# Kernel tuning notes

Hardware: AMD Instinct MI355X
Metric: run time of the kernel (lower is better)

## Reference

```python
import jax, jax.numpy as jnp
import numpy as np

NUM_BEAMS = 2


def setup_inputs() -> dict:
    key = jax.random.key(0)
    ks = jax.random.split(key, 5)
    B, T, H, E, F = 128, 32, 768, 4, 3072
    x = jax.random.normal(ks[0], (B, T, H), dtype=jnp.float32)
    Wg = jax.random.normal(ks[1], (E, H), dtype=jnp.float32) * (1.0 / np.sqrt(H))
    W1 = jax.random.normal(ks[2], (E, H, F), dtype=jnp.float32) * (1.0 / np.sqrt(H))
    b1 = jnp.zeros((E, F), dtype=jnp.float32)
    W2 = jax.random.normal(ks[3], (E, F, H), dtype=jnp.float32) * (1.0 / np.sqrt(F))
    b2 = jnp.zeros((E, H), dtype=jnp.float32)
    return {"x": x, "Wg": Wg, "W1": W1, "b1": b1, "W2": W2, "b2": b2}


def reference(x, Wg, W1, b1, W2, b2):
    B, T, H = x.shape
    E = Wg.shape[0]
    nb = NUM_BEAMS
    # ---- forward_gate: mask is all-ones, so masked mean == mean over tokens ----
    x_avg = jnp.mean(x, axis=1)                          # [B, H]
    logits_gate = x_avg @ Wg.T                           # [B, E]
    prob_gate = jax.nn.softmax(logits_gate, axis=-1)     # [B, E]
    # ---- importance auxiliary loss (torch.std uses ddof=1) ----
    importance = jnp.sum(prob_gate, axis=0)              # [E]
    importance_loss = (jnp.std(importance, ddof=1) / jnp.mean(importance)) ** 2
    # ---- beam search, first layer: exp(log(p)) == p, top-k per row ----
    current_scores = jnp.exp(jnp.log(prob_gate))         # == prob_gate (kept for fidelity)
    topk_values, gate_idx = jax.lax.top_k(current_scores, nb)   # [B, nb]
    beam_scores = topk_values.reshape(nb * B)            # row-major flatten, matches .view
    expert_route = gate_idx.reshape(nb * B)[:, None]     # [B*nb, 1]
    beam_idx = jnp.arange(nb * B)
    current_expert_select = expert_route[:, -1]          # [B*nb]
    # ---- first layer: replicate x and scores along beam dim (interleaved) ----
    x_rep = jnp.repeat(x, nb, axis=0)                    # [B*nb, T, H]
    scores_rep = jnp.repeat(prob_gate, nb, axis=0)       # [B*nb, E]
    # input_x = x_rep[beam_idx] is identity here (beam_idx == arange)
    # ---- forward_expert_ffn: run ALL experts, mask+combine with gate prob ----
    h1 = jnp.einsum('bth,ehf->betf', x_rep, W1) + b1[None, :, None, :]
    h1 = jax.nn.gelu(h1, approximate=False)              # torch GELU is exact erf form
    cand = jnp.einsum('betf,efh->beth', h1, W2) + b2[None, :, None, :]  # [B*nb, E, T, H]
    weight = scores_rep * jax.nn.one_hot(current_expert_select, E, dtype=scores_rep.dtype)
    output = jnp.einsum('beth,be->bth', cand, weight)    # weighted sum over experts
    return output, beam_scores, expert_route, beam_idx, importance_loss
```

## Files before the change

### kernel.cpp

```cpp
#include <hip/hip_runtime.h>
#include <math.h>

typedef _Float16 f16;
typedef _Float16 f16x8 __attribute__((ext_vector_type(8)));
typedef float f32x4 __attribute__((ext_vector_type(4)));

#define Bn 128
#define Tn 32
#define Hn 768
#define En 4
#define Fn 3072
#define Rn 256

static constexpr size_t OUT_ELEMS  = (size_t)Rn*Tn*Hn;
static constexpr size_t SCORES_OFF = OUT_ELEMS;
static constexpr size_t ROUTE_OFF  = OUT_ELEMS + Rn;
static constexpr size_t BIDX_OFF   = OUT_ELEMS + 2*Rn;
static constexpr size_t LOSS_OFF   = OUT_ELEMS + 3*Rn;

#define WS_WSF    0u
#define WS_ROUTE  4096u
#define WS_GRP    8192u
#define WS_X16    16384u
#define WS_W1T    (WS_X16 + 2u*Bn*Tn*Hn)
#define WS_W2T    (WS_W1T + 2u*En*Hn*Fn)
#define WS_H1     (WS_W2T + 2u*En*Fn*Hn)

#define GLOAD16(g, l) __builtin_amdgcn_global_load_lds( \
    (const __attribute__((address_space(1))) unsigned int*)(g), \
    (__attribute__((address_space(3))) unsigned int*)(l), 16, 0, 0)

__device__ __forceinline__ float fast_gelu(float v) {
  float s = v * 0.70710678118f;
  float a = fabsf(s);
  float t = 1.0f / (1.0f + 0.3275911f * a);
  float y = t*(0.254829592f + t*(-0.284496736f + t*(1.421413741f +
            t*(-1.453152027f + t*1.061405429f))));
  float er = 1.0f - y * __expf(-a*a);
  er = (s < 0.0f) ? -er : er;
  return 0.5f * v * (1.0f + er);
}

__global__ __launch_bounds__(256) void gate_kernel(
    const float* __restrict__ x, const float* __restrict__ Wg,
    float* __restrict__ out, float* __restrict__ wsf, int* __restrict__ route,
    f16* __restrict__ x16)
{
  const int b = blockIdx.x;
  const int tid = threadIdx.x;
  const int w = tid >> 6, l = tid & 63;
  __shared__ float pacc[4][4];
  float a0=0.f, a1=0.f, a2=0.f, a3=0.f;
  const float* xb = x   + (size_t)b*Tn*Hn + (size_t)(w*8)*Hn;
  f16*         xh = x16 + (size_t)b*Tn*Hn + (size_t)(w*8)*Hn;
  #pragma unroll
  for (int k = 0; k < 12; ++k) {
    const int h = l + 64*k;
    const float w0 = Wg[0*Hn+h], w1 = Wg[1*Hn+h], w2 = Wg[2*Hn+h], w3 = Wg[3*Hn+h];
    #pragma unroll
    for (int t = 0; t < 8; ++t) {
      float v = xb[t*Hn + h];
      xh[t*Hn + h] = (f16)v;
      a0 += v*w0; a1 += v*w1; a2 += v*w2; a3 += v*w3;
    }
  }
  #pragma unroll
  for (int o = 32; o > 0; o >>= 1) {
    a0 += __shfl_down(a0,o); a1 += __shfl_down(a1,o);
    a2 += __shfl_down(a2,o); a3 += __shfl_down(a3,o);
  }
  if (l == 0) { pacc[w][0]=a0; pacc[w][1]=a1; pacc[w][2]=a2; pacc[w][3]=a3; }
  __syncthreads();
  if (tid == 0) {
    float lg[4];
    #pragma unroll
    for (int e = 0; e < 4; ++e)
      lg[e] = (pacc[0][e]+pacc[1][e]+pacc[2][e]+pacc[3][e]) * (1.0f/Tn);
    float m = fmaxf(fmaxf(lg[0],lg[1]), fmaxf(lg[2],lg[3]));
    float p[4]; float s = 0.f;
    #pragma unroll
    for (int e = 0; e < 4; ++e) { p[e] = expf(lg[e]-m); s += p[e]; }
    float inv = 1.f/s;
    #pragma unroll
    for (int e = 0; e < 4; ++e) { p[e] *= inv; wsf[b*4+e] = p[e]; }
    int i1 = 0;
    #pragma unroll
    for (int e = 1; e < 4; ++e) if (p[e] > p[i1]) i1 = e;
    int i2 = (i1 == 0) ? 1 : 0;
    #pragma unroll
    for (int e = 0; e < 4; ++e) if (e != i1 && p[e] > p[i2]) i2 = e;
    int idx[2] = {i1, i2};
    #pragma unroll
    for (int k = 0; k < 2; ++k) {
      int r = 2*b + k;
      float pv = p[idx[k]];
      wsf[512 + r] = pv;
      route[r] = idx[k];
      out[SCORES_OFF + r] = pv;
      out[ROUTE_OFF  + r] = (float)idx[k];
      out[BIDX_OFF   + r] = (float)r;
    }
  }
}

__global__ __launch_bounds__(64) void loss_kernel(
    const float* __restrict__ wsf, float* __restrict__ out)
{
  const int l = threadIdx.x;
  float i0=0.f,i1=0.f,i2=0.f,i3=0.f;
  for (int b = l; b < Bn; b += 64) {
    i0 += wsf[b*4+0]; i1 += wsf[b*4+1]; i2 += wsf[b*4+2]; i3 += wsf[b*4+3];
  }
  #pragma unroll
  for (int o = 32; o > 0; o >>= 1) {
    i0 += __shfl_down(i0,o); i1 += __shfl_down(i1,o);
    i2 += __shfl_down(i2,o); i3 += __shfl_down(i3,o);
  }
  if (l == 0) {
    float mean = 0.25f*(i0+i1+i2+i3);
    float d0=i0-mean, d1=i1-mean, d2=i2-mean, d3=i3-mean;
    float var = (d0*d0+d1*d1+d2*d2+d3*d3) * (1.f/3.f);
    out[LOSS_OFF] = var / (mean*mean);
  }
}

__global__ __launch_bounds__(64) void group_kernel(
    const int* __restrict__ route, int* __restrict__ grp)
{
  const int l = threadIdx.x;
  int cnt = 0;
  if (l < 4) { for (int r = 0; r < Rn; ++r) cnt += (route[r] == l); }
  int c0 = __shfl(cnt, 0), c1 = __shfl(cnt, 1), c2 = __shfl(cnt, 2), c3 = __shfl(cnt, 3);
  int off = (l >= 1 ? c0 : 0) + (l >= 2 ? c1 : 0) + (l >= 3 ? c2 : 0);
  if (l < 4) {
    int p = off;
    for (int r = 0; r < Rn; ++r) if (route[r] == l) grp[384 + p++] = r;
  }
  if (l == 0) {
    int cs[4] = {c0, c1, c2, c3};
    int os[4] = {0, c0, c0+c1, c0+c1+c2};
    int nt4 = 0;
    for (int e = 0; e < 4; ++e) {
      for (int s = 0; s < cs[e]; s += 4) {
        int nb = cs[e] - s; if (nb > 4) nb = 4;
        grp[8+nt4*3+0] = e; grp[8+nt4*3+1] = os[e]+s; grp[8+nt4*3+2] = nb;
        ++nt4;
      }
    }
    grp[0] = nt4;
  }
}

__global__ __launch_bounds__(256) void transcvt_kernel(
    const float* __restrict__ W1s, const float* __restrict__ W2s,
    f16* __restrict__ d1, f16* __restrict__ d2)
{
  __shared__ f16 t[64][74];
  int bid = blockIdx.x;
  const float* s; f16* d; int R, C, rc;
  if (bid < 2304) { s = W1s; d = d1; R = Hn; C = Fn; rc = bid; }
  else            { s = W2s; d = d2; R = Fn; C = Hn; rc = bid - 2304; }
  const int e = rc / 576; rc -= e*576;
  const int nx = C >> 6;
  const int cy = rc / nx, cx = rc - cy*nx;
  const int r0 = cy*64, c0 = cx*64;
  s += (size_t)e*R*C;
  d += (size_t)e*R*C;
  const int tid = threadIdx.x;
  const int i  = tid >> 2;
  const int j0 = (tid & 3) * 16;
  #pragma unroll
  for (int q = 0; q < 16; q += 4) {
    float4 v = *(const float4*)(s + (size_t)(r0+i)*C + c0 + j0 + q);
    t[i][j0+q+0]=(f16)v.x; t[i][j0+q+1]=(f16)v.y; t[i][j0+q+2]=(f16)v.z; t[i][j0+q+3]=(f16)v.w;
  }
  __syncthreads();
  f16 o[16];
  #pragma unroll
  for (int q = 0; q < 16; ++q) o[q] = t[j0+q][i];
  *(uint4*)(d + (size_t)(c0+i)*R + r0 + j0)     = *(uint4*)&o[0];
  *(uint4*)(d + (size_t)(c0+i)*R + r0 + j0 + 8) = *(uint4*)&o[8];
}

template<int KD, int ND, int BN, int NWAVE, int NBUF, bool G1>
__global__ __launch_bounds__(NWAVE*64, 2) void gemm_kernel(
    const f16* __restrict__ A16, const f16* __restrict__ B16,
    const float* __restrict__ bias, f16* __restrict__ oh,
    float* __restrict__ of, const int* __restrict__ grp,
    const float* __restrict__ wsf)
{
  constexpr int NWY  = BN / 64;
  constexpr int NY   = ND / BN;
  constexpr int NT   = KD / 64;
  constexpr int GL_A = 1024 / (NWAVE*64);
  constexpr int GL_B = (BN*8) / (NWAVE*64);
  constexpr int NLD  = GL_A + GL_B;
  constexpr int BUFSZ = (128 + BN) * 128;
  constexpr int PRE_D = NBUF - 1;
  constexpr int TPR  = NWAVE*2;
  static_assert(NT % NBUF == 0, "NT % NBUF");

  const int ntiles = grp[0];
  const int njobs  = ntiles * NY;
  const int tid  = threadIdx.x;
  const int lane = tid & 63;
  const int w    = tid >> 6;

  extern __shared__ __align__(16) char smem[];

  const int wm = w / NWY, wn = w % NWY;
  const int lr = lane & 15, lk = lane >> 4;
  const int rowA0 = wm*64;
  const int rowB0 = wn*64;
  const int r7 = lr & 7;
  const int ub[2] = { ((lk) ^ r7) << 4, ((4+lk) ^ r7) << 4 };

  const int j0 = (int)(((long long)blockIdx.x     * njobs) / gridDim.x);
  const int j1 = (int)(((long long)(blockIdx.x+1) * njobs) / gridDim.x);

  for (int job = j0; job < j1; ++job) {
    const int tix = job / NY;
    const int ny  = job - tix*NY;
    const int e      = grp[8+tix*3+0];
    const int bstart = grp[8+tix*3+1];
    const int nb     = grp[8+tix*3+2];
    const int n0     = ny * BN;

    const f16* asrc[GL_A];
    #pragma unroll
    for (int i = 0; i < GL_A; ++i) {
      const int U   = (w*GL_A + i)*64 + lane;
      const int row = U >> 3;
      const int gu  = (U & 7) ^ (row & 7);
      int slot = row >> 5; if (slot >= nb) slot = nb - 1;
      const int beam = grp[384 + bstart + slot];
      const size_t rbase = (G1 ? (size_t)(beam>>1)*Tn : (size_t)beam*Tn) + (row & 31);
      asrc[i] = A16 + rbase*(size_t)KD + gu*8;
    }
    const f16* bsrc[GL_B];
    #pragma unroll
    for (int i = 0; i < GL_B; ++i) {
      const int U   = (w*GL_B + i)*64 + lane;
      const int row = U >> 3;
      const int gu  = (U & 7) ^ (row & 7);
      bsrc[i] = B16 + (size_t)e*ND*KD + (size_t)(n0 + row)*KD + gu*8;
    }

    f32x4 acc[4][4];
    #pragma unroll
    for (int i=0;i<4;++i)
      #pragma unroll
      for (int j=0;j<4;++j) acc[i][j] = (f32x4){0.f,0.f,0.f,0.f};

    auto STAGE = [&](int bsel, int kt2) {
      char* Ad = smem + bsel*BUFSZ + (w*GL_A)*1024;
      #pragma unroll
      for (int i = 0; i < GL_A; ++i) GLOAD16(asrc[i] + kt2*64, Ad + i*1024);
      char* Bd = smem + bsel*BUFSZ + 128*128 + (w*GL_B)*1024;
      #pragma unroll
      for (int i = 0; i < GL_B; ++i) GLOAD16(bsrc[i] + kt2*64, Bd + i*1024);
    };

#define PHASE(BUFI, KS, PRE, POST) do {                                        \
      const char* Ab_ = smem + (BUFI)*BUFSZ;                                   \
      const char* Bb_ = Ab_ + 128*128;                                         \
      f16x8 af[4], bf[4];                                                      \
      _Pragma("unroll")                                                        \
      for (int mi=0;mi<4;++mi)                                                 \
        af[mi] = *(const f16x8*)(Ab_ + (rowA0+mi*16+lr)*128 + ub[KS]);         \
      _Pragma("unroll")                                                        \
      for (int ni=0;ni<4;++ni)                                                 \
        bf[ni] = *(const f16x8*)(Bb_ + (rowB0+ni*16+lr)*128 + ub[KS]);         \
      PRE;                                                                     \
      __builtin_amdgcn_s_barrier();                                            \
      __builtin_amdgcn_sched_barrier(0);                                       \
      asm volatile("s_waitcnt lgkmcnt(0)" ::: "memory");                       \
      __builtin_amdgcn_sched_barrier(0);                                       \
      __builtin_amdgcn_s_setprio(1);                                           \
      _Pragma("unroll")                                                        \
      for (int mi=0;mi<4;++mi)                                                 \
        _Pragma("unroll")                                                      \
        for (int ni=0;ni<4;++ni)                                               \
          acc[mi][ni] = __builtin_amdgcn_mfma_f32_16x16x32_f16(af[mi], bf[ni], acc[mi][ni], 0, 0, 0); \
      __builtin_amdgcn_s_setprio(0);                                           \
      POST;                                                                    \
      __builtin_amdgcn_s_barrier();                                            \
      __builtin_amdgcn_sched_barrier(0);                                       \
    } while (0)

#define TILE(BUFI, KT) do {                                                    \
      PHASE(BUFI, 0,                                                           \
            { if ((KT)+PRE_D < NT) STAGE(((BUFI)+PRE_D)%NBUF, (KT)+PRE_D); },  \
            {});                                                               \
      PHASE(BUFI, 1, {},                                                       \
            { if (PRE_D == 2 && (KT)+2 < NT) {                                 \
                asm volatile("s_waitcnt vmcnt(%0)" :: "i"(NLD) : "memory");    \
              } else if ((KT)+1 < NT) {                                        \
                asm volatile("s_waitcnt vmcnt(0)" ::: "memory");               \
              }                                                                \
              __builtin_amdgcn_sched_barrier(0); });                           \
    } while (0)

    STAGE(0, 0);
    if (PRE_D == 2) {
      STAGE(1, 1);
      asm volatile("s_waitcnt vmcnt(%0)" :: "i"(NLD) : "memory");
    } else {
      asm volatile("s_waitcnt vmcnt(0)" ::: "memory");
    }
    __builtin_amdgcn_sched_barrier(0);
    __builtin_amdgcn_s_barrier();
    __builtin_amdgcn_sched_barrier(0);

    if constexpr (NBUF == 3) {
      for (int kt = 0; kt < NT; kt += 3) {
        TILE(0, kt);
        TILE(1, kt+1);
        TILE(2, kt+2);
      }
    } else {
      for (int kt = 0; kt < NT; kt += 2) {
        TILE(0, kt);
        TILE(1, kt+1);
      }
    }
#undef TILE
#undef PHASE

    const int nvalid = nb * Tn;
    char* cst = smem;
    float bvals[4];
    if (G1) {
      #pragma unroll
      for (int ni=0;ni<4;++ni) bvals[ni] = bias[e*ND + n0 + rowB0 + ni*16 + lr];
    }
    #pragma unroll
    for (int mi=0;mi<4;++mi){
      #pragma unroll
      for (int j=0;j<4;++j){
        const int m = rowA0 + mi*16 + (lane>>4)*4 + j;
        const int m7 = m & 7;
        #pragma unroll
        for (int ni=0;ni<4;++ni){
          const int n = rowB0 + ni*16 + lr;
          if (G1) {
            float v = acc[mi][ni][j] + bvals[ni];
            *(f16*)(cst + m*512 + (((n>>3)^m7)<<4) + (n&7)*2) = (f16)fast_gelu(v);
          } else {
            *(float*)(cst + m*512 + (((n>>2)^m7)<<4) + (n&3)*4) = acc[mi][ni][j];
          }
        }
      }
    }
    __syncthreads();
    {
      const int u  = tid & 31;
      const int tr = tid >> 5;
      float4 b4;
      if (!G1) b4 = *(const float4*)(bias + e*ND + n0 + u*4);
      #pragma unroll
      for (int it = 0; it < 128/TPR; ++it) {
        const int rl = it*TPR + tr;
        if (rl < nvalid) {
          const int beam = grp[384 + bstart + (rl>>5)];
          if (G1) {
            uint4 v = *(const uint4*)(cst + rl*512 + (((u&24)|((u&7)^(rl&7)))<<4));
            *(uint4*)(oh + ((size_t)beam*Tn + (rl&31))*(size_t)ND + n0 + u*8) = v;
          } else {
            const float sc = wsf[512 + beam];
            float4 v = *(const float4*)(cst + rl*512 + (((u&24)|((u&7)^(rl&7)))<<4));
            v.x = (v.x + b4.x)*sc; v.y = (v.y + b4.y)*sc;
            v.z = (v.z + b4.z)*sc; v.w = (v.w + b4.w)*sc;
            *(float4*)(of + ((size_t)beam*Tn + (rl&31))*(size_t)Hn + n0 + u*4) = v;
          }
        }
      }
    }
    __syncthreads();
  }
}

extern "C" void kernel_launch(void* const* d_in, const int* in_sizes, int n_in,
                              void* d_out, int out_size, void* d_ws, size_t ws_size,
                              hipStream_t stream)
{
  const float* x  = (const float*)d_in[0];
  const float* Wg = (const float*)d_in[1];
  const float* W1 = (const float*)d_in[2];
  const float* b1 = (const float*)d_in[3];
  const float* W2 = (const float*)d_in[4];
  const float* b2 = (const float*)d_in[5];
  float* out = (float*)d_out;
  char* ws = (char*)d_ws;
  float* wsf  = (float*)(ws + WS_WSF);
  int*   route= (int*)(ws + WS_ROUTE);
  int*   grp  = (int*)(ws + WS_GRP);
  f16*   x16  = (f16*)(ws + WS_X16);
  f16*   w1t  = (f16*)(ws + WS_W1T);
  f16*   w2t  = (f16*)(ws + WS_W2T);
  f16*   h1   = (f16*)(ws + WS_H1);

  gate_kernel<<<Bn, 256, 0, stream>>>(x, Wg, out, wsf, route, x16);
  group_kernel<<<1, 64, 0, stream>>>(route, grp);
  loss_kernel<<<1, 64, 0, stream>>>(wsf, out);
  transcvt_kernel<<<4608, 256, 0, stream>>>(W1, W2, w1t, w2t);

  auto g1 = gemm_kernel<Hn, Fn, 256, 8, 3, true>;
  auto g2 = gemm_kernel<Fn, Hn, 128, 4, 2, false>;
  const int sm1 = 3 * (128 + 256) * 128;
  const int sm2 = 2 * (128 + 128) * 128;
  hipFuncSetAttribute((const void*)g1, hipFuncAttributeMaxDynamicSharedMemorySize, sm1);
  hipFuncSetAttribute((const void*)g2, hipFuncAttributeMaxDynamicSharedMemorySize, sm2);
  g1<<<256, 512, sm1, stream>>>(x16, w1t, b1, h1, nullptr, grp, wsf);
  g2<<<512, 256, sm2, stream>>>(h1, w2t, b2, nullptr, out, grp, wsf);
}
```

Before: 231.8 us.

## Shrink GEMM K-tile to 32, drop persistent loop, one block per tile job

Both expert GEMMs now use a K step of 32 instead of 64, with a single-phase triple-buffered pipeline and a new XOR swizzle matched to 64-byte rows. Per-stage shared memory becomes much smaller, and G1's launch bounds request 4 blocks per CU to raise occupancy. The persistent job loop is replaced by a grid sized to the maximum tile count, with blocks past the real tile count exiting early. The trade-off is twice as many barriers and waits per K loop and a few idle blocks.

```diff
diff --git a/kernel.cpp b/kernel.cpp
--- a/kernel.cpp
+++ b/kernel.cpp
@@ -11,6 +11,7 @@
 #define En 4
 #define Fn 3072
 #define Rn 256
+#define MAXT4 67
 
 static constexpr size_t OUT_ELEMS  = (size_t)Rn*Tn*Hn;
 static constexpr size_t SCORES_OFF = OUT_ELEMS;
@@ -182,8 +183,8 @@
   *(uint4*)(d + (size_t)(c0+i)*R + r0 + j0 + 8) = *(uint4*)&o[8];
 }
 
-template<int KD, int ND, int BN, int NWAVE, int NBUF, bool G1>
-__global__ __launch_bounds__(NWAVE*64, 2) void gemm_kernel(
+template<int KD, int ND, int BN, int NWAVE, bool G1>
+__global__ __launch_bounds__(NWAVE*64, G1 ? 4 : 2) void gemm_kernel(
     const f16* __restrict__ A16, const f16* __restrict__ B16,
     const float* __restrict__ bias, f16* __restrict__ oh,
     float* __restrict__ of, const int* __restrict__ grp,
@@ -191,192 +192,166 @@
 {
   constexpr int NWY  = BN / 64;
   constexpr int NY   = ND / BN;
-  constexpr int NT   = KD / 64;
-  constexpr int GL_A = 1024 / (NWAVE*64);
-  constexpr int GL_B = (BN*8) / (NWAVE*64);
+  constexpr int NT   = KD / 32;
+  constexpr int NTHR = NWAVE * 64;
+  constexpr int GL_A = 512 / NTHR;
+  constexpr int GL_B = (BN*4) / NTHR;
   constexpr int NLD  = GL_A + GL_B;
-  constexpr int BUFSZ = (128 + BN) * 128;
-  constexpr int PRE_D = NBUF - 1;
-  constexpr int TPR  = NWAVE*2;
-  static_assert(NT % NBUF == 0, "NT % NBUF");
+  constexpr int BUFSZ = 8192 + BN*64;
+  constexpr int TPR  = NWAVE * 2;
+  static_assert(NT % 3 == 0, "NT%3");
 
   const int ntiles = grp[0];
-  const int njobs  = ntiles * NY;
-  const int tid  = threadIdx.x;
-  const int lane = tid & 63;
-  const int w    = tid >> 6;
+  const int tix = blockIdx.x / NY;
+  const int ny  = blockIdx.x % NY;
+  if (tix >= ntiles) return;
+  const int e      = grp[8+tix*3+0];
+  const int bstart = grp[8+tix*3+1];
+  const int nb     = grp[8+tix*3+2];
+  const int n0     = ny * BN;
+  const int tid    = threadIdx.x;
+  const int lane   = tid & 63;
+  const int w      = tid >> 6;
 
   extern __shared__ __align__(16) char smem[];
+
+  const f16* asrc[GL_A];
+  #pragma unroll
+  for (int i = 0; i < GL_A; ++i) {
+    const int U   = w*(GL_A*64) + i*64 + lane;
+    const int row = U >> 2;
+    const int gu  = (U & 3) ^ ((U >> 3) & 3);
+    int slot = row >> 5; if (slot >= nb) slot = nb - 1;
+    const int beam = grp[384 + bstart + slot];
+    const size_t rbase = (G1 ? (size_t)(beam>>1)*Tn : (size_t)beam*Tn) + (row & 31);
+    asrc[i] = A16 + rbase*(size_t)KD + gu*8;
+  }
+  const f16* bsrc[GL_B];
+  #pragma unroll
+  for (int i = 0; i < GL_B; ++i) {
+    const int U   = w*(GL_B*64) + i*64 + lane;
+    const int row = U >> 2;
+    const int gu  = (U & 3) ^ ((U >> 3) & 3);
+    bsrc[i] = B16 + (size_t)e*ND*KD + (size_t)(n0 + row)*KD + gu*8;
+  }
 
   const int wm = w / NWY, wn = w % NWY;
   const int lr = lane & 15, lk = lane >> 4;
   const int rowA0 = wm*64;
   const int rowB0 = wn*64;
-  const int r7 = lr & 7;
-  const int ub[2] = { ((lk) ^ r7) << 4, ((4+lk) ^ r7) << 4 };
-
-  const int j0 = (int)(((long long)blockIdx.x     * njobs) / gridDim.x);
-  const int j1 = (int)(((long long)(blockIdx.x+1) * njobs) / gridDim.x);
-
-  for (int job = j0; job < j1; ++job) {
-    const int tix = job / NY;
-    const int ny  = job - tix*NY;
-    const int e      = grp[8+tix*3+0];
-    const int bstart = grp[8+tix*3+1];
-    const int nb     = grp[8+tix*3+2];
-    const int n0     = ny * BN;
-
-    const f16* asrc[GL_A];
-    #pragma unroll
-    for (int i = 0; i < GL_A; ++i) {
-      const int U   = (w*GL_A + i)*64 + lane;
-      const int row = U >> 3;
-      const int gu  = (U & 7) ^ (row & 7);
-      int slot = row >> 5; if (slot >= nb) slot = nb - 1;
-      const int beam = grp[384 + bstart + slot];
-      const size_t rbase = (G1 ? (size_t)(beam>>1)*Tn : (size_t)beam*Tn) + (row & 31);
-      asrc[i] = A16 + rbase*(size_t)KD + gu*8;
-    }
-    const f16* bsrc[GL_B];
-    #pragma unroll
-    for (int i = 0; i < GL_B; ++i) {
-      const int U   = (w*GL_B + i)*64 + lane;
-      const int row = U >> 3;
-      const int gu  = (U & 7) ^ (row & 7);
-      bsrc[i] = B16 + (size_t)e*ND*KD + (size_t)(n0 + row)*KD + gu*8;
-    }
-
-    f32x4 acc[4][4];
-    #pragma unroll
-    for (int i=0;i<4;++i)
+  const int ub = (lk ^ ((lr >> 1) & 3)) << 4;
+
+  f32x4 acc[4][4];
+  #pragma unroll
+  for (int i=0;i<4;++i)
+    #pragma unroll
+    for (int j=0;j<4;++j) acc[i][j] = (f32x4){0.f,0.f,0.f,0.f};
+
+  auto STAGE = [&](int bsel, int kt2) {
+    char* Ad = smem + bsel*BUFSZ + (w*(GL_A*64))*16;
+    #pragma unroll
+    for (int i = 0; i < GL_A; ++i) GLOAD16(asrc[i] + kt2*32, Ad + i*1024);
+    char* Bd = smem + bsel*BUFSZ + 8192 + (w*(GL_B*64))*16;
+    #pragma unroll
+    for (int i = 0; i < GL_B; ++i) GLOAD16(bsrc[i] + kt2*32, Bd + i*1024);
+  };
+
+  auto TILE = [&](int k, int b, bool dost, int vmc) {
+    const char* Ab = smem + b*BUFSZ;
+    const char* Bb = Ab + 8192;
+    f16x8 af[4], bf[4];
+    #pragma unroll
+    for (int mi=0;mi<4;++mi)
+      af[mi] = *(const f16x8*)(Ab + (rowA0 + mi*16 + lr)*64 + ub);
+    #pragma unroll
+    for (int ni=0;ni<4;++ni)
+      bf[ni] = *(const f16x8*)(Bb + (rowB0 + ni*16 + lr)*64 + ub);
+    if (dost) STAGE((b+2)%3, k+2);
+    __builtin_amdgcn_sched_barrier(0);
+    __builtin_amdgcn_s_barrier();
+    __builtin_amdgcn_sched_barrier(0);
+    asm volatile("s_waitcnt lgkmcnt(0)" ::: "memory");
+    __builtin_amdgcn_sched_barrier(0);
+    __builtin_amdgcn_s_setprio(1);
+    #pragma unroll
+    for (int mi=0;mi<4;++mi)
       #pragma unroll
-      for (int j=0;j<4;++j) acc[i][j] = (f32x4){0.f,0.f,0.f,0.f};
-
-    auto STAGE = [&](int bsel, int kt2) {
-      char* Ad = smem + bsel*BUFSZ + (w*GL_A)*1024;
+      for (int ni=0;ni<4;++ni)
+        acc[mi][ni] = __builtin_amdgcn_mfma_f32_16x16x32_f16(af[mi], bf[ni], acc[mi][ni], 0, 0, 0);
+    __builtin_amdgcn_s_setprio(0);
+    if (vmc > 0)       asm volatile("s_waitcnt vmcnt(%0)" :: "i"(NLD) : "memory");
+    else if (vmc == 0) asm volatile("s_waitcnt vmcnt(0)" ::: "memory");
+    __builtin_amdgcn_sched_barrier(0);
+    __builtin_amdgcn_s_barrier();
+    __builtin_amdgcn_sched_barrier(0);
+  };
+
+  STAGE(0, 0);
+  STAGE(1, 1);
+  asm volatile("s_waitcnt vmcnt(%0)" :: "i"(NLD) : "memory");
+  __builtin_amdgcn_sched_barrier(0);
+  __builtin_amdgcn_s_barrier();
+  __builtin_amdgcn_sched_barrier(0);
+
+  {
+    int b = 0;
+    for (int k = 0; k < NT-2; ++k) {
+      TILE(k, b, true, NLD);
+      b = (b+1)%3;
+    }
+    TILE(NT-2, b, false, 0);
+    b = (b+1)%3;
+    TILE(NT-1, b, false, -1);
+  }
+
+  const int nvalid = nb * Tn;
+  char* cst = smem;
+  float bvals[4];
+  if (G1) {
+    #pragma unroll
+    for (int ni=0;ni<4;++ni) bvals[ni] = bias[e*ND + n0 + rowB0 + ni*16 + lr];
+  }
+  #pragma unroll
+  for (int mi=0;mi<4;++mi){
+    #pragma unroll
+    for (int j=0;j<4;++j){
+      const int m = rowA0 + mi*16 + (lane>>4)*4 + j;
+      const int m7 = m & 7;
       #pragma unroll
-      for (int i = 0; i < GL_A; ++i) GLOAD16(asrc[i] + kt2*64, Ad + i*1024);
-      char* Bd = smem + bsel*BUFSZ + 128*128 + (w*GL_B)*1024;
-      #pragma unroll
-      for (int i = 0; i < GL_B; ++i) GLOAD16(bsrc[i] + kt2*64, Bd + i*1024);
-    };
-
-#define PHASE(BUFI, KS, PRE, POST) do {                                        \
-      const char* Ab_ = smem + (BUFI)*BUFSZ;                                   \
-      const char* Bb_ = Ab_ + 128*128;                                         \
-      f16x8 af[4], bf[4];                                                      \
-      _Pragma("unroll")                                                        \
-      for (int mi=0;mi<4;++mi)                                                 \
-        af[mi] = *(const f16x8*)(Ab_ + (rowA0+mi*16+lr)*128 + ub[KS]);         \
-      _Pragma("unroll")                                                        \
-      for (int ni=0;ni<4;++ni)                                                 \
-        bf[ni] = *(const f16x8*)(Bb_ + (rowB0+ni*16+lr)*128 + ub[KS]);         \
-      PRE;                                                                     \
-      __builtin_amdgcn_s_barrier();                                            \
-      __builtin_amdgcn_sched_barrier(0);                                       \
-      asm volatile("s_waitcnt lgkmcnt(0)" ::: "memory");                       \
-      __builtin_amdgcn_sched_barrier(0);                                       \
-      __builtin_amdgcn_s_setprio(1);                                           \
-      _Pragma("unroll")                                                        \
-      for (int mi=0;mi<4;++mi)                                                 \
-        _Pragma("unroll")                                                      \
-        for (int ni=0;ni<4;++ni)                                               \
-          acc[mi][ni] = __builtin_amdgcn_mfma_f32_16x16x32_f16(af[mi], bf[ni], acc[mi][ni], 0, 0, 0); \
-      __builtin_amdgcn_s_setprio(0);                                           \
-      POST;                                                                    \
-      __builtin_amdgcn_s_barrier();                                            \
-      __builtin_amdgcn_sched_barrier(0);                                       \
-    } while (0)
-
-#define TILE(BUFI, KT) do {                                                    \
-      PHASE(BUFI, 0,                                                           \
-            { if ((KT)+PRE_D < NT) STAGE(((BUFI)+PRE_D)%NBUF, (KT)+PRE_D); },  \
-            {});                                                               \
-      PHASE(BUFI, 1, {},                                                       \
-            { if (PRE_D == 2 && (KT)+2 < NT) {                                 \
-                asm volatile("s_waitcnt vmcnt(%0)" :: "i"(NLD) : "memory");    \
-              } else if ((KT)+1 < NT) {                                        \
-                asm volatile("s_waitcnt vmcnt(0)" ::: "memory");               \
-              }                                                                \
-              __builtin_amdgcn_sched_barrier(0); });                           \
-    } while (0)
-
-    STAGE(0, 0);
-    if (PRE_D == 2) {
-      STAGE(1, 1);
-      asm volatile("s_waitcnt vmcnt(%0)" :: "i"(NLD) : "memory");
-    } else {
-      asm volatile("s_waitcnt vmcnt(0)" ::: "memory");
-    }
-    __builtin_amdgcn_sched_barrier(0);
-    __builtin_amdgcn_s_barrier();
-    __builtin_amdgcn_sched_barrier(0);
-
-    if constexpr (NBUF == 3) {
-      for (int kt = 0; kt < NT; kt += 3) {
-        TILE(0, kt);
-        TILE(1, kt+1);
-        TILE(2, kt+2);
-      }
-    } else {
-      for (int kt = 0; kt < NT; kt += 2) {
-        TILE(0, kt);
-        TILE(1, kt+1);
-      }
-    }
-#undef TILE
-#undef PHASE
-
-    const int nvalid = nb * Tn;
-    char* cst = smem;
-    float bvals[4];
-    if (G1) {
-      #pragma unroll
-      for (int ni=0;ni<4;++ni) bvals[ni] = bias[e*ND + n0 + rowB0 + ni*16 + lr];
-    }
-    #pragma unroll
-    for (int mi=0;mi<4;++mi){
-      #pragma unroll
-      for (int j=0;j<4;++j){
-        const int m = rowA0 + mi*16 + (lane>>4)*4 + j;
-        const int m7 = m & 7;
-        #pragma unroll
-        for (int ni=0;ni<4;++ni){
-          const int n = rowB0 + ni*16 + lr;
-          if (G1) {
-            float v = acc[mi][ni][j] + bvals[ni];
-            *(f16*)(cst + m*512 + (((n>>3)^m7)<<4) + (n&7)*2) = (f16)fast_gelu(v);
-          } else {
-            *(float*)(cst + m*512 + (((n>>2)^m7)<<4) + (n&3)*4) = acc[mi][ni][j];
-          }
+      for (int ni=0;ni<4;++ni){
+        const int n = rowB0 + ni*16 + lr;
+        if (G1) {
+          float v = acc[mi][ni][j] + bvals[ni];
+          *(f16*)(cst + m*512 + (((n>>3)^m7)<<4) + (n&7)*2) = (f16)fast_gelu(v);
+        } else {
+          *(float*)(cst + m*512 + (((n>>2)^m7)<<4) + (n&3)*4) = acc[mi][ni][j];
         }
       }
     }
-    __syncthreads();
-    {
-      const int u  = tid & 31;
-      const int tr = tid >> 5;
-      float4 b4;
-      if (!G1) b4 = *(const float4*)(bias + e*ND + n0 + u*4);
-      #pragma unroll
-      for (int it = 0; it < 128/TPR; ++it) {
-        const int rl = it*TPR + tr;
-        if (rl < nvalid) {
-          const int beam = grp[384 + bstart + (rl>>5)];
-          if (G1) {
-            uint4 v = *(const uint4*)(cst + rl*512 + (((u&24)|((u&7)^(rl&7)))<<4));
-            *(uint4*)(oh + ((size_t)beam*Tn + (rl&31))*(size_t)ND + n0 + u*8) = v;
-          } else {
-            const float sc = wsf[512 + beam];
-            float4 v = *(const float4*)(cst + rl*512 + (((u&24)|((u&7)^(rl&7)))<<4));
-            v.x = (v.x + b4.x)*sc; v.y = (v.y + b4.y)*sc;
-            v.z = (v.z + b4.z)*sc; v.w = (v.w + b4.w)*sc;
-            *(float4*)(of + ((size_t)beam*Tn + (rl&31))*(size_t)Hn + n0 + u*4) = v;
-          }
+  }
+  __syncthreads();
+  {
+    const int u  = tid & 31;
+    const int tr = tid >> 5;
+    float4 b4;
+    if (!G1) b4 = *(const float4*)(bias + e*ND + n0 + u*4);
+    #pragma unroll
+    for (int it = 0; it < 128/TPR; ++it) {
+      const int rl = it*TPR + tr;
+      if (rl < nvalid) {
+        const int beam = grp[384 + bstart + (rl>>5)];
+        if (G1) {
+          uint4 v = *(const uint4*)(cst + rl*512 + (((u&24)|((u&7)^(rl&7)))<<4));
+          *(uint4*)(oh + ((size_t)beam*Tn + (rl&31))*(size_t)ND + n0 + u*8) = v;
+        } else {
+          const float sc = wsf[512 + beam];
+          float4 v = *(const float4*)(cst + rl*512 + (((u&24)|((u&7)^(rl&7)))<<4));
+          v.x = (v.x + b4.x)*sc; v.y = (v.y + b4.y)*sc;
+          v.z = (v.z + b4.z)*sc; v.w = (v.w + b4.w)*sc;
+          *(float4*)(of + ((size_t)beam*Tn + (rl&31))*(size_t)Hn + n0 + u*4) = v;
         }
       }
     }
-    __syncthreads();
   }
 }
 
@@ -405,12 +380,12 @@
   loss_kernel<<<1, 64, 0, stream>>>(wsf, out);
   transcvt_kernel<<<4608, 256, 0, stream>>>(W1, W2, w1t, w2t);
 
-  auto g1 = gemm_kernel<Hn, Fn, 256, 8, 3, true>;
-  auto g2 = gemm_kernel<Fn, Hn, 128, 4, 2, false>;
-  const int sm1 = 3 * (128 + 256) * 128;
-  const int sm2 = 2 * (128 + 128) * 128;
+  auto g1 = gemm_kernel<Hn, Fn, 256, 8, true>;
+  auto g2 = gemm_kernel<Fn, Hn, 128, 4, false>;
+  const int sm1 = 3*(8192 + 256*64);
+  const int sm2 = 65536;
   hipFuncSetAttribute((const void*)g1, hipFuncAttributeMaxDynamicSharedMemorySize, sm1);
   hipFuncSetAttribute((const void*)g2, hipFuncAttributeMaxDynamicSharedMemorySize, sm2);
-  g1<<<256, 512, sm1, stream>>>(x16, w1t, b1, h1, nullptr, grp, wsf);
-  g2<<<512, 256, sm2, stream>>>(h1, w2t, b2, nullptr, out, grp, wsf);
-}
+  g1<<<MAXT4*12, 512, sm1, stream>>>(x16, w1t, b1, h1, nullptr, grp, wsf);
+  g2<<<MAXT4*6,  256, sm2, stream>>>(h1, w2t, b2, nullptr, out, grp, wsf);
+}
```

Measured after the change: 204.7 us. 11.7% less time.
